# Performance work log

Measured on AMD Instinct MI355X. Metric: run time of the kernel, lower is better.

Reference implementation:

```python
import jax, jax.numpy as jnp
import numpy as np

B, S, H, D = 8, 1024, 16, 64
EMBED_DIM = H * D  # 1024
NEG_INF = -1e30


def setup_inputs() -> dict:
    key = jax.random.key(0)
    kq, kk, kv, kl = jax.random.split(key, 4)
    q = jax.random.normal(kq, (B, S, H, D), dtype=jnp.float32)
    k = jax.random.normal(kk, (B, S, H, D), dtype=jnp.float32)
    v = jax.random.normal(kv, (B, S, H, D), dtype=jnp.float32)
    # ragged lengths in [S//4, S]; prefix-style key_padding_mask (True = valid)
    lengths = jax.random.randint(kl, (B,), S // 4, S + 1)
    key_padding_mask = jnp.arange(S)[None, :] < lengths[:, None]
    return {"q": q, "k": k, "v": v, "key_padding_mask": key_padding_mask}


def reference(q, k, v, key_padding_mask):
    # Equivalent math of flash_attn_unpadded_qkvpacked_func on unpadded tokens
    # followed by pad_input (zeros at padded query rows), dropout=0 (eval).
    # NOTE: module uses softmax_scale = embed_dim ** -0.5 (not head_dim).
    scale = EMBED_DIM ** (-0.5)
    scores = jnp.einsum("bqhd,bkhd->bhqk", q, k) * scale  # [B,H,S,S]
    scores = jnp.where(key_padding_mask[:, None, None, :], scores, NEG_INF)
    attn = jax.nn.softmax(scores, axis=-1)
    out = jnp.einsum("bhqk,bkhd->bqhd", attn, v)  # [B,S,H,D]
    # pad_input re-inserts zeros at padded query positions
    out = out * key_padding_mask[:, :, None, None].astype(out.dtype)
    return out.reshape(B, S, H * D)
```

## Files before the change

kernel.cpp:

```cpp
#include <hip/hip_runtime.h>


#define SS 1024
#define NH 16
#define DD 64
#define ROWSTRIDE (NH * DD)
#define SCALE 0.03125f
#define LOG2E 1.4426950408889634f
#define PC1 (SCALE * LOG2E)
#define PC2 (-12.0f * LOG2E)
#define KSTR 72
#define VSTR 72

typedef short bf16x8 __attribute__((ext_vector_type(8)));
typedef unsigned short u16;
typedef unsigned short u16x8 __attribute__((ext_vector_type(8)));
typedef unsigned short u16x4 __attribute__((ext_vector_type(4)));
typedef float f32x4 __attribute__((ext_vector_type(4)));
typedef unsigned u32x4 __attribute__((ext_vector_type(4)));

__device__ __forceinline__ u16 f2bf(float x) {
  unsigned u = __builtin_bit_cast(unsigned, x);
  return (u16)((u + 0x7FFFu + ((u >> 16) & 1u)) >> 16);
}
__device__ __forceinline__ float bf2f(u16 s) {
  unsigned u = ((unsigned)s) << 16;
  return __builtin_bit_cast(float, u);
}
__device__ __forceinline__ unsigned pkbf(float a, float b) {
#if __has_builtin(__builtin_amdgcn_cvt_pk_bf16_f32)
  auto r = __builtin_amdgcn_cvt_pk_bf16_f32(a, b);
  return __builtin_bit_cast(unsigned, r);
#else
  return (unsigned)f2bf(a) | ((unsigned)f2bf(b) << 16);
#endif
}

__global__ __launch_bounds__(256, 4) void fa_main(const void* qv, const void* kv,
                                                  const void* vv, const void* maskv,
                                                  float* out) {
  __shared__ __attribute__((aligned(16))) u16 Kt[2][64 * KSTR];
  __shared__ __attribute__((aligned(16))) u16 Vt[2][64 * VSTR + 64];

  int tid = threadIdx.x;
  int lane = tid & 63;
  int w = tid >> 6;
  int t = lane & 15;
  int quad = lane >> 4;

  int bid = blockIdx.x;
  int x = bid & 7;
  int j = bid >> 3;
  int g = j >> 4;
  int r = j & 15;
  int qt = (r + g) & 15;
  int bh = (g << 3) + x;
  int h = bh & (NH - 1);
  int b = bh >> 4;
  int q0 = qt * 64;

  const u16* qs16 = (const u16*)qv;
  float dv = bf2f(qs16[2 * lane]);
  unsigned long long bal = __ballot(!(fabsf(dv) < 100.0f));
  int isf32 = (__popcll(bal) >= 16) ? 1 : 0;

  const unsigned char* m8 = (const unsigned char*)maskv;
  const int* m32 = (const int*)maskv;
  bool isu8 = (m8[1] != 0);
  int lo = 0, hi = SS;
  while (lo < hi) {
    int mid = (lo + hi) >> 1;
    int vbit = isu8 ? (m8[b * SS + mid] != 0) : (m32[b * SS + mid] != 0);
    if (vbit) lo = mid + 1; else hi = mid;
  }
  int len = lo;

  size_t base = (size_t)b * SS * ROWSTRIDE + h * DD;

  if (q0 >= len) {
    f32x4 z4 = {0.f, 0.f, 0.f, 0.f};
    for (int i = tid; i < 64 * 16; i += 256) {
      int r2 = i >> 4, dseg = (i & 15) << 2;
      *(f32x4*)&out[base + (size_t)(q0 + r2) * ROWSTRIDE + dseg] = z4;
    }
    return;
  }

  int qrow = q0 + w * 16 + t;
  bf16x8 qf[2];
  if (isf32) {
    const float* qp = (const float*)qv + base + (size_t)qrow * ROWSTRIDE + quad * 8;
#pragma unroll
    for (int kk = 0; kk < 2; kk++) {
      union { bf16x8 v; unsigned d[4]; } u;
#pragma unroll
      for (int jj = 0; jj < 4; jj++)
        u.d[jj] = pkbf(qp[kk * 32 + 2 * jj], qp[kk * 32 + 2 * jj + 1]);
      qf[kk] = u.v;
    }
  } else {
    const u16* qp = (const u16*)qv + base + (size_t)qrow * ROWSTRIDE + quad * 8;
#pragma unroll
    for (int kk = 0; kk < 2; kk++) qf[kk] = *(const bf16x8*)(qp + kk * 32);
  }

  f32x4 zero4 = {0.f, 0.f, 0.f, 0.f};
  f32x4 oacc[4];
#pragma unroll
  for (int c = 0; c < 4; c++) oacc[c] = zero4;
  float lsum = 0.f;

  int key = tid >> 2, seg = tid & 3;
  int kp = tid >> 3, ds = tid & 7;
  int nkt = (len + 63) >> 6;

  f32x4 kA[4], vA[4];
  u16x8 kB[2], vB[2];

  auto issue_loads = [&](int kt) {
    int krow = kt * 64 + key;
    if (krow > SS - 1) krow = SS - 1;
    int vrow = kt * 64 + 2 * kp;
    if (vrow > SS - 2) vrow = SS - 2;
    size_t ksrc = base + (size_t)krow * ROWSTRIDE + seg * 16;
    size_t vsrc = base + (size_t)vrow * ROWSTRIDE + ds * 8;
    if (isf32) {
      const f32x4* kpp = (const f32x4*)((const float*)kv + ksrc);
#pragma unroll
      for (int i = 0; i < 4; i++) kA[i] = kpp[i];
      const float* vp = (const float*)vv + vsrc;
      vA[0] = *(const f32x4*)vp;
      vA[1] = *(const f32x4*)(vp + 4);
      vA[2] = *(const f32x4*)(vp + ROWSTRIDE);
      vA[3] = *(const f32x4*)(vp + ROWSTRIDE + 4);
    } else {
      const u16x8* kpp = (const u16x8*)((const u16*)kv + ksrc);
      kB[0] = kpp[0]; kB[1] = kpp[1];
      const u16* vp = (const u16*)vv + vsrc;
      vB[0] = *(const u16x8*)vp;
      vB[1] = *(const u16x8*)(vp + ROWSTRIDE);
    }
  };

  auto stage_to_lds = [&](int bsel) {
    u16* KtB = &Kt[bsel][0];
    u16* VtB = &Vt[bsel][0];
    if (isf32) {
      unsigned kd[8];
#pragma unroll
      for (int i = 0; i < 8; i++)
        kd[i] = pkbf(kA[i >> 1][2 * (i & 1)], kA[i >> 1][2 * (i & 1) + 1]);
      *(u32x4*)&KtB[key * KSTR + seg * 16] = u32x4{kd[0], kd[1], kd[2], kd[3]};
      *(u32x4*)&KtB[key * KSTR + seg * 16 + 8] = u32x4{kd[4], kd[5], kd[6], kd[7]};
#pragma unroll
      for (int jj = 0; jj < 8; jj++) {
        int d = ds * 8 + jj;
        *(unsigned*)&VtB[d * VSTR + (d >> 4) * 16 + 2 * kp] =
            pkbf(vA[jj >> 2][jj & 3], vA[2 + (jj >> 2)][jj & 3]);
      }
    } else {
      *(u16x8*)&KtB[key * KSTR + seg * 16] = kB[0];
      *(u16x8*)&KtB[key * KSTR + seg * 16 + 8] = kB[1];
#pragma unroll
      for (int jj = 0; jj < 8; jj++) {
        int d = ds * 8 + jj;
        *(unsigned*)&VtB[d * VSTR + (d >> 4) * 16 + 2 * kp] =
            (unsigned)(u16)vB[0][jj] | ((unsigned)(u16)vB[1][jj] << 16);
      }
    }
  };

  issue_loads(0);
  stage_to_lds(0);
  if (nkt > 1) issue_loads(1);
  __syncthreads();

  for (int kt = 0; kt < nkt; ++kt) {
    int cur = kt & 1, nxt = cur ^ 1;
    if (kt + 1 < nkt) stage_to_lds(nxt);
    if (kt + 2 < nkt) issue_loads(kt + 2);

    const u16* KtC = &Kt[cur][0];
    const u16* VtC = &Vt[cur][0];

    f32x4 sacc[4];
#pragma unroll
    for (int c = 0; c < 4; c++) sacc[c] = zero4;
    __builtin_amdgcn_s_setprio(1);
#pragma unroll
    for (int kk = 0; kk < 2; kk++) {
#pragma unroll
      for (int c = 0; c < 4; c++) {
        bf16x8 ka = *(const bf16x8*)&KtC[(c * 16 + t) * KSTR + kk * 32 + quad * 8];
        sacc[c] = __builtin_amdgcn_mfma_f32_16x16x32_bf16(ka, qf[kk], sacc[c], 0, 0, 0);
      }
    }
    __builtin_amdgcn_s_setprio(0);

    float p[4][4];
    if (kt == nkt - 1) {
      int krem = len - kt * 64;
#pragma unroll
      for (int c = 0; c < 4; c++) {
        int kbase = c * 16 + quad * 4;
#pragma unroll
        for (int rr = 0; rr < 4; rr++)
          p[c][rr] = (kbase + rr < krem)
                         ? __builtin_amdgcn_exp2f(fmaf(sacc[c][rr], PC1, PC2))
                         : 0.0f;
      }
    } else {
#pragma unroll
      for (int c = 0; c < 4; c++)
#pragma unroll
        for (int rr = 0; rr < 4; rr++)
          p[c][rr] = __builtin_amdgcn_exp2f(fmaf(sacc[c][rr], PC1, PC2));
    }
#pragma unroll
    for (int c = 0; c < 4; c++)
      lsum += (p[c][0] + p[c][1]) + (p[c][2] + p[c][3]);

    unsigned pd[4][2];
#pragma unroll
    for (int c = 0; c < 4; c++) {
      pd[c][0] = pkbf(p[c][0], p[c][1]);
      pd[c][1] = pkbf(p[c][2], p[c][3]);
    }

    __builtin_amdgcn_s_setprio(1);
#pragma unroll
    for (int kc = 0; kc < 2; kc++) {
      union { bf16x8 v; unsigned d[4]; } pa;
      pa.d[0] = pd[2 * kc][0];
      pa.d[1] = pd[2 * kc][1];
      pa.d[2] = pd[2 * kc + 1][0];
      pa.d[3] = pd[2 * kc + 1][1];
#pragma unroll
      for (int c = 0; c < 4; c++) {
        const u16* vr = &VtC[(c * 16 + t) * VSTR + c * 16 + kc * 32 + quad * 4];
        union { bf16x8 v; u16x4 h[2]; } vb;
        vb.h[0] = *(const u16x4*)vr;
        vb.h[1] = *(const u16x4*)(vr + 16);
        oacc[c] = __builtin_amdgcn_mfma_f32_16x16x32_bf16(pa.v, vb.v, oacc[c], 0, 0, 0);
      }
    }
    __builtin_amdgcn_s_setprio(0);

    __syncthreads();
  }

  lsum += __shfl_xor(lsum, 16);
  lsum += __shfl_xor(lsum, 32);
  float inv[4];
#pragma unroll
  for (int rr = 0; rr < 4; rr++)
    inv[rr] = 1.0f / __shfl(lsum, quad * 4 + rr);
#pragma unroll
  for (int c = 0; c < 4; c++)
#pragma unroll
    for (int rr = 0; rr < 4; rr++) {
      int qr = q0 + w * 16 + quad * 4 + rr;
      float o = oacc[c][rr] * inv[rr];
      out[base + (size_t)qr * ROWSTRIDE + c * 16 + t] = (qr < len) ? o : 0.0f;
    }
}

extern "C" void kernel_launch(void* const* d_in, const int* in_sizes, int n_in,
                              void* d_out, int out_size, void* d_ws, size_t ws_size,
                              hipStream_t stream) {
  fa_main<<<2048, 256, 0, stream>>>(d_in[0], d_in[1], d_in[2], d_in[3], (float*)d_out);
}
```

Before: 170.1 us.

## Halve key tile to 32 and split K/V loading across thread halves

Shrinks the key/value tile from 64 to 32 keys per iteration. Threads 0-127 now load and stage K while threads 128-255 load and stage V, so each thread keeps half the staging registers. The s_setprio hints around the MFMA blocks are removed. The aim is lower register and LDS use, which may allow more resident blocks, at the cost of twice as many loop iterations and __syncthreads barriers per tile.

```diff
diff --git a/kernel.cpp b/kernel.cpp
--- a/kernel.cpp
+++ b/kernel.cpp
@@ -10,7 +10,7 @@
 #define PC1 (SCALE * LOG2E)
 #define PC2 (-12.0f * LOG2E)
 #define KSTR 72
-#define VSTR 72
+#define VSTR 40
 
 typedef short bf16x8 __attribute__((ext_vector_type(8)));
 typedef unsigned short u16;
@@ -39,7 +39,7 @@
 __global__ __launch_bounds__(256, 4) void fa_main(const void* qv, const void* kv,
                                                   const void* vv, const void* maskv,
                                                   float* out) {
-  __shared__ __attribute__((aligned(16))) u16 Kt[2][64 * KSTR];
+  __shared__ __attribute__((aligned(16))) u16 Kt[2][32 * KSTR];
   __shared__ __attribute__((aligned(16))) u16 Vt[2][64 * VSTR + 64];
 
   int tid = threadIdx.x;
@@ -110,62 +110,76 @@
   for (int c = 0; c < 4; c++) oacc[c] = zero4;
   float lsum = 0.f;
 
+  int nkt = (len + 31) >> 5;
+
+  bool isK = tid < 128;
   int key = tid >> 2, seg = tid & 3;
-  int kp = tid >> 3, ds = tid & 7;
-  int nkt = (len + 63) >> 6;
-
-  f32x4 kA[4], vA[4];
-  u16x8 kB[2], vB[2];
+  int u2 = tid - 128, kp = u2 >> 3, ds = u2 & 7;
+
+  f32x4 sA[4];
+  u16x8 sB[2];
 
   auto issue_loads = [&](int kt) {
-    int krow = kt * 64 + key;
-    if (krow > SS - 1) krow = SS - 1;
-    int vrow = kt * 64 + 2 * kp;
-    if (vrow > SS - 2) vrow = SS - 2;
-    size_t ksrc = base + (size_t)krow * ROWSTRIDE + seg * 16;
-    size_t vsrc = base + (size_t)vrow * ROWSTRIDE + ds * 8;
-    if (isf32) {
-      const f32x4* kpp = (const f32x4*)((const float*)kv + ksrc);
-#pragma unroll
-      for (int i = 0; i < 4; i++) kA[i] = kpp[i];
-      const float* vp = (const float*)vv + vsrc;
-      vA[0] = *(const f32x4*)vp;
-      vA[1] = *(const f32x4*)(vp + 4);
-      vA[2] = *(const f32x4*)(vp + ROWSTRIDE);
-      vA[3] = *(const f32x4*)(vp + ROWSTRIDE + 4);
+    if (isK) {
+      int krow = kt * 32 + key;
+      if (krow > SS - 1) krow = SS - 1;
+      size_t ksrc = base + (size_t)krow * ROWSTRIDE + seg * 16;
+      if (isf32) {
+        const f32x4* kpp = (const f32x4*)((const float*)kv + ksrc);
+#pragma unroll
+        for (int i = 0; i < 4; i++) sA[i] = kpp[i];
+      } else {
+        const u16x8* kpp = (const u16x8*)((const u16*)kv + ksrc);
+        sB[0] = kpp[0]; sB[1] = kpp[1];
+      }
     } else {
-      const u16x8* kpp = (const u16x8*)((const u16*)kv + ksrc);
-      kB[0] = kpp[0]; kB[1] = kpp[1];
-      const u16* vp = (const u16*)vv + vsrc;
-      vB[0] = *(const u16x8*)vp;
-      vB[1] = *(const u16x8*)(vp + ROWSTRIDE);
+      int vrow = kt * 32 + 2 * kp;
+      if (vrow > SS - 2) vrow = SS - 2;
+      size_t vsrc = base + (size_t)vrow * ROWSTRIDE + ds * 8;
+      if (isf32) {
+        const float* vp = (const float*)vv + vsrc;
+        sA[0] = *(const f32x4*)vp;
+        sA[1] = *(const f32x4*)(vp + 4);
+        sA[2] = *(const f32x4*)(vp + ROWSTRIDE);
+        sA[3] = *(const f32x4*)(vp + ROWSTRIDE + 4);
+      } else {
+        const u16* vp = (const u16*)vv + vsrc;
+        sB[0] = *(const u16x8*)vp;
+        sB[1] = *(const u16x8*)(vp + ROWSTRIDE);
+      }
     }
   };
 
   auto stage_to_lds = [&](int bsel) {
-    u16* KtB = &Kt[bsel][0];
-    u16* VtB = &Vt[bsel][0];
-    if (isf32) {
-      unsigned kd[8];
-#pragma unroll
-      for (int i = 0; i < 8; i++)
-        kd[i] = pkbf(kA[i >> 1][2 * (i & 1)], kA[i >> 1][2 * (i & 1) + 1]);
-      *(u32x4*)&KtB[key * KSTR + seg * 16] = u32x4{kd[0], kd[1], kd[2], kd[3]};
-      *(u32x4*)&KtB[key * KSTR + seg * 16 + 8] = u32x4{kd[4], kd[5], kd[6], kd[7]};
-#pragma unroll
-      for (int jj = 0; jj < 8; jj++) {
-        int d = ds * 8 + jj;
-        *(unsigned*)&VtB[d * VSTR + (d >> 4) * 16 + 2 * kp] =
-            pkbf(vA[jj >> 2][jj & 3], vA[2 + (jj >> 2)][jj & 3]);
+    if (isK) {
+      u16* KtB = &Kt[bsel][0];
+      if (isf32) {
+        unsigned kd[8];
+#pragma unroll
+        for (int i = 0; i < 8; i++)
+          kd[i] = pkbf(sA[i >> 1][2 * (i & 1)], sA[i >> 1][2 * (i & 1) + 1]);
+        *(u32x4*)&KtB[key * KSTR + seg * 16] = u32x4{kd[0], kd[1], kd[2], kd[3]};
+        *(u32x4*)&KtB[key * KSTR + seg * 16 + 8] = u32x4{kd[4], kd[5], kd[6], kd[7]};
+      } else {
+        *(u16x8*)&KtB[key * KSTR + seg * 16] = sB[0];
+        *(u16x8*)&KtB[key * KSTR + seg * 16 + 8] = sB[1];
       }
     } else {
-      *(u16x8*)&KtB[key * KSTR + seg * 16] = kB[0];
-      *(u16x8*)&KtB[key * KSTR + seg * 16 + 8] = kB[1];
-#pragma unroll
-      for (int jj = 0; jj < 8; jj++) {
-        int d = ds * 8 + jj;
-        *(unsigned*)&VtB[d * VSTR + (d >> 4) * 16 + 2 * kp] =
-            (unsigned)(u16)vB[0][jj] | ((unsigned)(u16)vB[1][jj] << 16);
+      u16* VtB = &Vt[bsel][0];
+      if (isf32) {
+#pragma unroll
+        for (int jj = 0; jj < 8; jj++) {
+          int d = ds * 8 + jj;
+          *(unsigned*)&VtB[d * VSTR + (d >> 4) * 16 + 2 * kp] =
+              pkbf(sA[jj >> 2][jj & 3], sA[2 + (jj >> 2)][jj & 3]);
+        }
+      } else {
+#pragma unroll
+        for (int jj = 0; jj < 8; jj++) {
+          int d = ds * 8 + jj;
+          *(unsigned*)&VtB[d * VSTR + (d >> 4) * 16 + 2 * kp] =
+              (unsigned)(u16)sB[0][jj] | ((unsigned)(u16)sB[1][jj] << 16);
+        }
       }
     }
   };
@@ -183,68 +197,53 @@
     const u16* KtC = &Kt[cur][0];
     const u16* VtC = &Vt[cur][0];
 
-    f32x4 sacc[4];
-#pragma unroll
-    for (int c = 0; c < 4; c++) sacc[c] = zero4;
-    __builtin_amdgcn_s_setprio(1);
+    f32x4 sacc[2];
+    sacc[0] = zero4; sacc[1] = zero4;
 #pragma unroll
     for (int kk = 0; kk < 2; kk++) {
 #pragma unroll
-      for (int c = 0; c < 4; c++) {
+      for (int c = 0; c < 2; c++) {
         bf16x8 ka = *(const bf16x8*)&KtC[(c * 16 + t) * KSTR + kk * 32 + quad * 8];
         sacc[c] = __builtin_amdgcn_mfma_f32_16x16x32_bf16(ka, qf[kk], sacc[c], 0, 0, 0);
       }
     }
-    __builtin_amdgcn_s_setprio(0);
-
-    float p[4][4];
-    if (kt == nkt - 1) {
-      int krem = len - kt * 64;
-#pragma unroll
-      for (int c = 0; c < 4; c++) {
-        int kbase = c * 16 + quad * 4;
+
+    unsigned pd[2][2];
+    bool lastt = (kt == nkt - 1);
+    int krem = len - kt * 32;
+#pragma unroll
+    for (int c = 0; c < 2; c++) {
+      int kbase = c * 16 + quad * 4;
+      float p[4];
+      if (lastt) {
 #pragma unroll
         for (int rr = 0; rr < 4; rr++)
-          p[c][rr] = (kbase + rr < krem)
-                         ? __builtin_amdgcn_exp2f(fmaf(sacc[c][rr], PC1, PC2))
-                         : 0.0f;
-      }
-    } else {
-#pragma unroll
-      for (int c = 0; c < 4; c++)
+          p[rr] = (kbase + rr < krem)
+                      ? __builtin_amdgcn_exp2f(fmaf(sacc[c][rr], PC1, PC2))
+                      : 0.0f;
+      } else {
 #pragma unroll
         for (int rr = 0; rr < 4; rr++)
-          p[c][rr] = __builtin_amdgcn_exp2f(fmaf(sacc[c][rr], PC1, PC2));
-    }
-#pragma unroll
-    for (int c = 0; c < 4; c++)
-      lsum += (p[c][0] + p[c][1]) + (p[c][2] + p[c][3]);
-
-    unsigned pd[4][2];
+          p[rr] = __builtin_amdgcn_exp2f(fmaf(sacc[c][rr], PC1, PC2));
+      }
+      lsum += (p[0] + p[1]) + (p[2] + p[3]);
+      pd[c][0] = pkbf(p[0], p[1]);
+      pd[c][1] = pkbf(p[2], p[3]);
+    }
+
+    union { bf16x8 v; unsigned d[4]; } pa;
+    pa.d[0] = pd[0][0];
+    pa.d[1] = pd[0][1];
+    pa.d[2] = pd[1][0];
+    pa.d[3] = pd[1][1];
 #pragma unroll
     for (int c = 0; c < 4; c++) {
-      pd[c][0] = pkbf(p[c][0], p[c][1]);
-      pd[c][1] = pkbf(p[c][2], p[c][3]);
-    }
-
-    __builtin_amdgcn_s_setprio(1);
-#pragma unroll
-    for (int kc = 0; kc < 2; kc++) {
-      union { bf16x8 v; unsigned d[4]; } pa;
-      pa.d[0] = pd[2 * kc][0];
-      pa.d[1] = pd[2 * kc][1];
-      pa.d[2] = pd[2 * kc + 1][0];
-      pa.d[3] = pd[2 * kc + 1][1];
-#pragma unroll
-      for (int c = 0; c < 4; c++) {
-        const u16* vr = &VtC[(c * 16 + t) * VSTR + c * 16 + kc * 32 + quad * 4];
-        union { bf16x8 v; u16x4 h[2]; } vb;
-        vb.h[0] = *(const u16x4*)vr;
-        vb.h[1] = *(const u16x4*)(vr + 16);
-        oacc[c] = __builtin_amdgcn_mfma_f32_16x16x32_bf16(pa.v, vb.v, oacc[c], 0, 0, 0);
-      }
-    }
-    __builtin_amdgcn_s_setprio(0);
+      const u16* vr = &VtC[(c * 16 + t) * VSTR + c * 16 + quad * 4];
+      union { bf16x8 v; u16x4 hh[2]; } vb;
+      vb.hh[0] = *(const u16x4*)vr;
+      vb.hh[1] = *(const u16x4*)(vr + 16);
+      oacc[c] = __builtin_amdgcn_mfma_f32_16x16x32_bf16(pa.v, vb.v, oacc[c], 0, 0, 0);
+    }
 
     __syncthreads();
   }
```

New measurement: 165.7 us. 2.6% less time.
